# Optimization experiments

Measured on AMD Instinct MI355X. Metric: run time of the kernel, lower is better.

The kernel has to match this reference:

```python
import jax, jax.numpy as jnp
import numpy as np

DECAY = 0.97
TEMP = 0.7
EPS = 1e-6
NORM_EPS = 1e-12  # torch F.normalize default eps


def _l2norm(x, axis=-1):
    n = jnp.linalg.norm(x, axis=axis, keepdims=True)
    return x / jnp.maximum(n, NORM_EPS)


def setup_inputs() -> dict:
    key = jax.random.key(0)
    k1, k2, k3 = jax.random.split(key, 3)
    pair_embed = jax.random.normal(k1, (8, 2048, 1024), dtype=jnp.float32)
    patterns = _l2norm(jax.random.normal(k2, (4096, 1024), dtype=jnp.float32))
    usage = jax.random.uniform(k3, (4096,), dtype=jnp.float32)
    return {"pair_embed": pair_embed, "patterns": patterns, "usage": usage}


def reference(pair_embed, patterns, usage):
    G, D = patterns.shape
    flat = pair_embed.reshape(-1, D)                      # [N, D]
    queries = _l2norm(flat)
    pat_n = _l2norm(patterns)
    logits = queries @ pat_n.T                             # [N, G]
    homeostasis = jnp.log(jnp.clip(usage, EPS))
    weights = jax.nn.softmax((logits - homeostasis[None, :]) / TEMP, axis=-1)

    # Hebbian EMA update (mirrors update(); no_grad in original)
    flat_assign = weights                                  # [N, G]
    weights_sum = flat_assign.sum(axis=0)                  # [G]
    valid = weights_sum > 0
    usage_new = usage * DECAY
    usage_new = jnp.where(valid, usage_new + (1.0 - DECAY) * weights_sum, usage_new)
    updates = flat_assign.T @ flat                         # [G, D]
    updates = updates / (weights_sum[:, None] + EPS)
    blended = _l2norm(patterns * DECAY + (1.0 - DECAY) * updates)
    patterns_new = jnp.where(valid[:, None], blended, patterns)

    out_weights = weights.reshape(*pair_embed.shape[:-1], G)
    return out_weights, patterns_new, usage_new
```

## Files before the change

kernel.cpp:

```cpp
#include <hip/hip_runtime.h>
#include <stdint.h>
#include <math.h>


#define DECAY 0.97f
#define OMD 0.03f
#define INV_TEMP (1.0f / 0.7f)
#define EPS 1e-6f
#define NORM_EPS 1e-12f

constexpr int NROWS = 16384;
constexpr int DK = 1024;
constexpr int GP = 4096;

typedef unsigned short u16;
typedef __bf16 bf16x8 __attribute__((ext_vector_type(8)));
typedef float f32x4 __attribute__((ext_vector_type(4)));

__device__ inline u16 f2bf(float x) {
    union { float f; uint32_t u; } c; c.f = x;
    uint32_t r = c.u + 0x7fffu + ((c.u >> 16) & 1u);
    return (u16)(r >> 16);
}

__device__ inline void gl_lds16(const u16* g, u16* l) {
    __builtin_amdgcn_global_load_lds(
        (const __attribute__((address_space(1))) void*)g,
        (__attribute__((address_space(3))) void*)l, 16, 0, 0);
}

__global__ __launch_bounds__(256) void norm_rows_kernel(
        const float* __restrict__ in, u16* __restrict__ outn) {
    __shared__ float sred[4];
    const int row = blockIdx.x;
    const int t = threadIdx.x;
    const float4 v = ((const float4*)(in + (size_t)row * DK))[t];
    float ss = v.x * v.x + v.y * v.y + v.z * v.z + v.w * v.w;
#pragma unroll
    for (int o = 32; o > 0; o >>= 1) ss += __shfl_xor(ss, o);
    if ((t & 63) == 0) sred[t >> 6] = ss;
    __syncthreads();
    const float tot = sred[0] + sred[1] + sred[2] + sred[3];
    const float rs = 1.0f / fmaxf(sqrtf(tot), NORM_EPS);
    ushort4 o4;
    o4.x = f2bf(v.x * rs); o4.y = f2bf(v.y * rs);
    o4.z = f2bf(v.z * rs); o4.w = f2bf(v.w * rs);
    ((ushort4*)(outn + (size_t)row * DK))[t] = o4;
}

__global__ __launch_bounds__(256) void prep_scalars_kernel(
        const float* __restrict__ usage, float* __restrict__ hscaled,
        float* __restrict__ wsum, float* __restrict__ rowsum) {
    const int i = blockIdx.x * 256 + threadIdx.x;
    if (i < GP) {
        hscaled[i] = logf(fmaxf(usage[i], EPS)) * INV_TEMP;
        wsum[i] = 0.0f;
    }
    rowsum[i] = 0.0f;
}

__global__ __launch_bounds__(256) void rowinv_kernel(float* __restrict__ rowsum) {
    const int i = blockIdx.x * 256 + threadIdx.x;
    rowsum[i] = 1.0f / rowsum[i];
}

__global__ __launch_bounds__(256) void zero_kernel(float4* __restrict__ p) {
    p[(size_t)blockIdx.x * 256 + threadIdx.x] = (float4){0.f, 0.f, 0.f, 0.f};
}

__global__ __launch_bounds__(256) void transpose_f32_bf16_kernel(
        const float* __restrict__ in, u16* __restrict__ out, int R, int C) {
    __shared__ float tile[64][260];
    const int r0 = blockIdx.x * 64;
    const int c0 = blockIdx.y * 256;
    const int t = threadIdx.x;
    const int fr = t & 63;
    const int rr = t >> 6;
#pragma unroll
    for (int j = 0; j < 16; ++j) {
        const int r = rr + 4 * j;
        const float4 v = *(const float4*)(in + (size_t)(r0 + r) * C + c0 + fr * 4);
        *(float4*)&tile[r][fr * 4] = v;
    }
    __syncthreads();
    __align__(16) u16 tmp[64];
#pragma unroll
    for (int r = 0; r < 64; ++r) tmp[r] = f2bf(tile[r][t]);
    u16* op = out + (size_t)(c0 + t) * R + r0;
#pragma unroll
    for (int i = 0; i < 8; ++i) ((uint4*)op)[i] = ((const uint4*)tmp)[i];
}

__global__ __launch_bounds__(256) void scale_transpose_kernel(
        float* __restrict__ W, const float* __restrict__ invs,
        u16* __restrict__ wT, float* __restrict__ wsum) {
    __shared__ float tile[64][260];
    __shared__ float sinv[64];
    const int r0 = blockIdx.x * 64;
    const int c0 = blockIdx.y * 256;
    const int t = threadIdx.x;
    if (t < 64) sinv[t] = invs[r0 + t];
    __syncthreads();
    const int fr = t & 63;
    const int rr = t >> 6;
#pragma unroll
    for (int j = 0; j < 16; ++j) {
        const int r = rr + 4 * j;
        float4 v = *(const float4*)(W + (size_t)(r0 + r) * GP + c0 + fr * 4);
        const float s = sinv[r];
        v.x *= s; v.y *= s; v.z *= s; v.w *= s;
        *(float4*)(W + (size_t)(r0 + r) * GP + c0 + fr * 4) = v;
        *(float4*)&tile[r][fr * 4] = v;
    }
    __syncthreads();
    __align__(16) u16 tmp[64];
    float csum = 0.f;
#pragma unroll
    for (int r = 0; r < 64; ++r) {
        const float x = tile[r][t];
        csum += x;
        tmp[r] = f2bf(x);
    }
    u16* op = wT + (size_t)(c0 + t) * NROWS + r0;
#pragma unroll
    for (int i = 0; i < 8; ++i) ((uint4*)op)[i] = ((const uint4*)tmp)[i];
    atomicAdd(&wsum[c0 + t], csum);
}

template <int KSTEPS, int KLD>
__device__ inline void gemm_bt_256x256(const u16* __restrict__ A,
                                       const u16* __restrict__ B,
                                       int m0, int n0, int k0,
                                       u16* sm, f32x4 acc[8][4]) {
    constexpr int SLOT = 32768;
    constexpr int BOFF = 16384;
    const int t = threadIdx.x;
    const int lane = t & 63;
    const int wave = t >> 6;
    const int wm = (wave >> 2) * 128;
    const int wn = (wave & 3) * 64;
    const int fr = lane & 15;
    const int q8 = lane >> 4;

    const int srow = 32 * wave + (lane >> 3);
    const int soct = (lane & 7) ^ (srow & 7);
    const size_t a_base = (size_t)(m0 + srow) * KLD + k0 + soct * 8;
    const size_t b_base = (size_t)(n0 + srow) * KLD + k0 + soct * 8;

    auto STAGE = [&](int slot, int kt) {
        u16* sa = sm + slot * SLOT;
        u16* sb = sa + BOFF;
#pragma unroll
        for (int i = 0; i < 4; ++i) {
            gl_lds16(A + a_base + (size_t)(8 * i) * KLD + kt,
                     sa + (32 * wave + 8 * i) * 64);
            gl_lds16(B + b_base + (size_t)(8 * i) * KLD + kt,
                     sb + (32 * wave + 8 * i) * 64);
        }
    };

    STAGE(0, 0);
    asm volatile("s_waitcnt vmcnt(0)" ::: "memory");
    __builtin_amdgcn_sched_barrier(0);
    __builtin_amdgcn_s_barrier();
    __builtin_amdgcn_sched_barrier(0);

    int slot = 0;
#pragma unroll 1
    for (int kt = 0; kt < KSTEPS; kt += 64) {
        if (kt + 64 < KSTEPS) STAGE(slot ^ 1, kt + 64);
        const u16* sa = sm + slot * SLOT;
        const u16* sb = sa + BOFF;
#pragma unroll
        for (int ks8 = 0; ks8 < 8; ks8 += 4) {
            bf16x8 af[8], bfr[4];
#pragma unroll
            for (int f = 0; f < 8; ++f) {
                const int ra = wm + f * 16 + fr;
                af[f]  = *(const bf16x8*)(sa + ra * 64 + (((ks8 + q8) ^ (ra & 7)) * 8));
            }
#pragma unroll
            for (int f = 0; f < 4; ++f) {
                const int rb = wn + f * 16 + fr;
                bfr[f] = *(const bf16x8*)(sb + rb * 64 + (((ks8 + q8) ^ (rb & 7)) * 8));
            }
            __builtin_amdgcn_s_setprio(1);
#pragma unroll
            for (int fm = 0; fm < 8; ++fm)
#pragma unroll
                for (int fn = 0; fn < 4; ++fn)
                    acc[fm][fn] = __builtin_amdgcn_mfma_f32_16x16x32_bf16(
                        af[fm], bfr[fn], acc[fm][fn], 0, 0, 0);
            __builtin_amdgcn_s_setprio(0);
        }
        if (kt + 64 < KSTEPS) {
            asm volatile("s_waitcnt vmcnt(0)" ::: "memory");
            __builtin_amdgcn_sched_barrier(0);
            __builtin_amdgcn_s_barrier();
            __builtin_amdgcn_sched_barrier(0);
        }
        slot ^= 1;
    }
}

__global__ __launch_bounds__(512, 2) void gemm1_kernel(
        const u16* __restrict__ Q, const u16* __restrict__ P,
        const float* __restrict__ hs, float* __restrict__ Wout,
        float* __restrict__ rowsum) {
    __shared__ u16 sm[2 * 32768];
    const int bid = blockIdx.x;
    const int m0 = (bid >> 4) * 256;
    const int n0 = (bid & 15) * 256;
    f32x4 acc[8][4];
#pragma unroll
    for (int a = 0; a < 8; ++a)
#pragma unroll
        for (int b = 0; b < 4; ++b) acc[a][b] = (f32x4){0.f, 0.f, 0.f, 0.f};
    gemm_bt_256x256<DK, DK>(Q, P, m0, n0, 0, sm, acc);

    const int lane = threadIdx.x & 63;
    const int wave = threadIdx.x >> 6;
    const int wm = (wave >> 2) * 128, wn = (wave & 3) * 64;
    const int cq = lane & 15, rq = (lane >> 4) * 4;
    float hval[4];
#pragma unroll
    for (int fn = 0; fn < 4; ++fn) hval[fn] = hs[n0 + wn + fn * 16 + cq];
#pragma unroll
    for (int fm = 0; fm < 8; ++fm) {
        const int mb = m0 + wm + fm * 16 + rq;
#pragma unroll
        for (int r = 0; r < 4; ++r) {
            float rs = 0.f;
#pragma unroll
            for (int fn = 0; fn < 4; ++fn) {
                const int g = n0 + wn + fn * 16 + cq;
                const float e = __expf(acc[fm][fn][r] * INV_TEMP - hval[fn]);
                Wout[(size_t)(mb + r) * GP + g] = e;
                rs += e;
            }
#pragma unroll
            for (int o = 1; o < 16; o <<= 1) rs += __shfl_xor(rs, o);
            if (cq == 0) atomicAdd(&rowsum[mb + r], rs);
        }
    }
}

__global__ __launch_bounds__(512, 2) void gemm2_kernel(
        const u16* __restrict__ WT, const u16* __restrict__ FT,
        float* __restrict__ Upart) {
    __shared__ u16 sm[2 * 32768];
    const int bid = blockIdx.x;
    const int k0 = (bid & 3) * 4096;
    const int n0 = ((bid >> 2) & 3) * 256;
    const int m0 = (bid >> 4) * 256;
    f32x4 acc[8][4];
#pragma unroll
    for (int a = 0; a < 8; ++a)
#pragma unroll
        for (int b = 0; b < 4; ++b) acc[a][b] = (f32x4){0.f, 0.f, 0.f, 0.f};
    gemm_bt_256x256<4096, NROWS>(WT, FT, m0, n0, k0, sm, acc);

    const int lane = threadIdx.x & 63;
    const int wave = threadIdx.x >> 6;
    const int wm = (wave >> 2) * 128, wn = (wave & 3) * 64;
    const int cq = lane & 15, rq = (lane >> 4) * 4;
#pragma unroll
    for (int fn = 0; fn < 4; ++fn) {
        const int d = n0 + wn + fn * 16 + cq;
#pragma unroll
        for (int fm = 0; fm < 8; ++fm) {
            const int gb = m0 + wm + fm * 16 + rq;
#pragma unroll
            for (int r = 0; r < 4; ++r)
                atomicAdd(&Upart[(size_t)(gb + r) * DK + d], acc[fm][fn][r]);
        }
    }
}

__global__ __launch_bounds__(256) void usage_kernel(
        const float* __restrict__ usage, const float* __restrict__ wsum,
        float* __restrict__ Uout, float* __restrict__ invw) {
    const int g = blockIdx.x * 256 + threadIdx.x;
    if (g < GP) {
        const float s = wsum[g];
        Uout[g] = usage[g] * DECAY + (s > 0.f ? OMD * s : 0.f);
        invw[g] = 1.0f / (s + EPS);
    }
}

__global__ __launch_bounds__(256) void finalize_patterns_kernel(
        const float* __restrict__ patterns, const float* __restrict__ wsum,
        const float* __restrict__ invw, const float* __restrict__ Upart,
        float* __restrict__ Pout) {
    __shared__ float sred[4];
    const int g = blockIdx.x;
    const int t = threadIdx.x;
    const float iw = invw[g] * OMD;
    const float4 u4 = ((const float4*)(Upart + (size_t)g * DK))[t];
    const float4 p4 = ((const float4*)(patterns + (size_t)g * DK))[t];
    float4 b;
    b.x = DECAY * p4.x + iw * u4.x;
    b.y = DECAY * p4.y + iw * u4.y;
    b.z = DECAY * p4.z + iw * u4.z;
    b.w = DECAY * p4.w + iw * u4.w;
    float ss = b.x * b.x + b.y * b.y + b.z * b.z + b.w * b.w;
#pragma unroll
    for (int o = 32; o > 0; o >>= 1) ss += __shfl_xor(ss, o);
    if ((t & 63) == 0) sred[t >> 6] = ss;
    __syncthreads();
    const float tot = sred[0] + sred[1] + sred[2] + sred[3];
    const float rs = 1.0f / fmaxf(sqrtf(tot), NORM_EPS);
    float4 o4;
    if (wsum[g] > 0.f) {
        o4.x = b.x * rs; o4.y = b.y * rs; o4.z = b.z * rs; o4.w = b.w * rs;
    } else {
        o4 = p4;
    }
    ((float4*)(Pout + (size_t)g * DK))[t] = o4;
}

extern "C" void kernel_launch(void* const* d_in, const int* in_sizes, int n_in,
                              void* d_out, int out_size, void* d_ws, size_t ws_size,
                              hipStream_t stream) {
    const float* pair_embed = (const float*)d_in[0];
    const float* patterns   = (const float*)d_in[1];
    const float* usage      = (const float*)d_in[2];

    float* out_w = (float*)d_out;
    float* out_p = out_w + (size_t)NROWS * GP;
    float* out_u = out_p + (size_t)GP * DK;

    char* ws = (char*)d_ws;
    u16* q_bf   = (u16*)(ws);
    float* Upart = (float*)(ws);
    u16* pat_bf = (u16*)(ws + 33554432);
    u16* fT     = (u16*)(ws + 41943040);
    u16* wT     = (u16*)(ws + 75497472);
    float* hs   = (float*)(ws + 209715200);
    float* wsum = (float*)(ws + 209715200 + 16384);
    float* invw = (float*)(ws + 209715200 + 32768);
    float* rsum = (float*)(ws + 209715200 + 49152);

    prep_scalars_kernel<<<64, 256, 0, stream>>>(usage, hs, wsum, rsum);
    norm_rows_kernel<<<NROWS, 256, 0, stream>>>(pair_embed, q_bf);
    norm_rows_kernel<<<GP, 256, 0, stream>>>(patterns, pat_bf);
    {
        dim3 g(NROWS / 64, DK / 256);
        transpose_f32_bf16_kernel<<<g, 256, 0, stream>>>(pair_embed, fT, NROWS, DK);
    }
    gemm1_kernel<<<(NROWS / 256) * (GP / 256), 512, 0, stream>>>(q_bf, pat_bf, hs, out_w, rsum);
    rowinv_kernel<<<64, 256, 0, stream>>>(rsum);
    {
        dim3 g(NROWS / 64, GP / 256);
        scale_transpose_kernel<<<g, 256, 0, stream>>>(out_w, rsum, wT, wsum);
    }
    usage_kernel<<<16, 256, 0, stream>>>(usage, wsum, out_u, invw);
    zero_kernel<<<(GP * DK / 4) / 256, 256, 0, stream>>>((float4*)Upart);
    gemm2_kernel<<<4 * (GP / 256) * (DK / 256), 512, 0, stream>>>(wT, fT, Upart);
    finalize_patterns_kernel<<<GP, 256, 0, stream>>>(patterns, wsum, invw, Upart, out_p);
}
```

Measured before the change: 826.6 us.

## Split GEMM main loop into four barrier-synced LDS-load/MFMA phases

Restructures the 256x256 bf16 GEMM inner loop into four phases. Each phase loads half the A fragments (and B when needed) from LDS, synchronizes the workgroup with a barrier plus lgkmcnt wait, then issues 16 MFMAs. This halves the live A-fragment registers and aims to interleave waves' LDS reads and MFMA work, in the style of ping-pong scheduling with two blocks per CU. It adds several extra workgroup barriers per k-step, which could stall waves if the phases don't line up well.

```diff
diff --git a/kernel.cpp b/kernel.cpp
--- a/kernel.cpp
+++ b/kernel.cpp
@@ -159,6 +159,35 @@
         }
     };
 
+#define LDA4(ks8, mh) do {                                                     \
+    _Pragma("unroll")                                                          \
+    for (int f = 0; f < 4; ++f) {                                              \
+        const int ra = wm + ((mh) * 4 + f) * 16 + fr;                          \
+        af[f] = *(const bf16x8*)(sa + ra * 64 + ((((ks8) + q8) ^ (ra & 7)) * 8)); \
+    } } while (0)
+
+#define LDB4(ks8) do {                                                         \
+    _Pragma("unroll")                                                          \
+    for (int f = 0; f < 4; ++f) {                                              \
+        const int rb = wn + f * 16 + fr;                                       \
+        bfr[f] = *(const bf16x8*)(sb + rb * 64 + ((((ks8) + q8) ^ (rb & 7)) * 8)); \
+    } } while (0)
+
+#define MFMA16(mh) do {                                                        \
+    __builtin_amdgcn_s_setprio(1);                                             \
+    _Pragma("unroll")                                                          \
+    for (int f = 0; f < 4; ++f)                                                \
+        _Pragma("unroll")                                                      \
+        for (int fn = 0; fn < 4; ++fn)                                         \
+            acc[(mh) * 4 + f][fn] = __builtin_amdgcn_mfma_f32_16x16x32_bf16(   \
+                af[f], bfr[fn], acc[(mh) * 4 + f][fn], 0, 0, 0);               \
+    __builtin_amdgcn_s_setprio(0); } while (0)
+
+#define PHASE_SYNC() do {                                                      \
+    __builtin_amdgcn_s_barrier();                                              \
+    asm volatile("s_waitcnt lgkmcnt(0)" ::: "memory");                         \
+    __builtin_amdgcn_sched_barrier(0); } while (0)
+
     STAGE(0, 0);
     asm volatile("s_waitcnt vmcnt(0)" ::: "memory");
     __builtin_amdgcn_sched_barrier(0);
@@ -168,39 +197,41 @@
     int slot = 0;
 #pragma unroll 1
     for (int kt = 0; kt < KSTEPS; kt += 64) {
-        if (kt + 64 < KSTEPS) STAGE(slot ^ 1, kt + 64);
         const u16* sa = sm + slot * SLOT;
         const u16* sb = sa + BOFF;
-#pragma unroll
-        for (int ks8 = 0; ks8 < 8; ks8 += 4) {
-            bf16x8 af[8], bfr[4];
-#pragma unroll
-            for (int f = 0; f < 8; ++f) {
-                const int ra = wm + f * 16 + fr;
-                af[f]  = *(const bf16x8*)(sa + ra * 64 + (((ks8 + q8) ^ (ra & 7)) * 8));
-            }
-#pragma unroll
-            for (int f = 0; f < 4; ++f) {
-                const int rb = wn + f * 16 + fr;
-                bfr[f] = *(const bf16x8*)(sb + rb * 64 + (((ks8 + q8) ^ (rb & 7)) * 8));
-            }
-            __builtin_amdgcn_s_setprio(1);
-#pragma unroll
-            for (int fm = 0; fm < 8; ++fm)
-#pragma unroll
-                for (int fn = 0; fn < 4; ++fn)
-                    acc[fm][fn] = __builtin_amdgcn_mfma_f32_16x16x32_bf16(
-                        af[fm], bfr[fn], acc[fm][fn], 0, 0, 0);
-            __builtin_amdgcn_s_setprio(0);
-        }
-        if (kt + 64 < KSTEPS) {
-            asm volatile("s_waitcnt vmcnt(0)" ::: "memory");
-            __builtin_amdgcn_sched_barrier(0);
-            __builtin_amdgcn_s_barrier();
-            __builtin_amdgcn_sched_barrier(0);
-        }
+        const bool next = (kt + 64 < KSTEPS);
+        bf16x8 af[4], bfr[4];
+
+        if (next) STAGE(slot ^ 1, kt + 64);
+        LDA4(0, 0); LDB4(0);
+        PHASE_SYNC();
+        MFMA16(0);
+        __builtin_amdgcn_s_barrier();
+
+        LDA4(0, 1);
+        PHASE_SYNC();
+        MFMA16(1);
+        __builtin_amdgcn_s_barrier();
+
+        LDA4(4, 0); LDB4(4);
+        PHASE_SYNC();
+        MFMA16(0);
+        __builtin_amdgcn_s_barrier();
+
+        LDA4(4, 1);
+        PHASE_SYNC();
+        MFMA16(1);
+        if (next) asm volatile("s_waitcnt vmcnt(0)" ::: "memory");
+        __builtin_amdgcn_sched_barrier(0);
+        __builtin_amdgcn_s_barrier();
+        __builtin_amdgcn_sched_barrier(0);
+
         slot ^= 1;
     }
+#undef LDA4
+#undef LDB4
+#undef MFMA16
+#undef PHASE_SYNC
 }
 
 __global__ __launch_bounds__(512, 2) void gemm1_kernel(
```

Result: slower. 845.6 us (+2.3%).

## Restructure GEMM mainloop into 4-slot 32-wide K pipeline with 3-deep prefetch

Applied to the files above, without the earlier changes.

The shared 256x256 GEMM mainloop changes from a two-slot double buffer with 64-wide K tiles to a four-slot ring of 32-wide K tiles, with three stages in flight. It waits with partial vmcnt counts so only the oldest stage must land before each barrier. The LDS swizzle and staging addressing are rewritten for 32-element rows. The aim is to hide global-to-LDS latency better and drop the full vmcnt(0) drain each iteration, at the cost of twice as many barriers per K and more complex waitcnt bookkeeping.

```diff
diff --git a/kernel.cpp b/kernel.cpp
--- a/kernel.cpp
+++ b/kernel.cpp
@@ -132,8 +132,9 @@
                                        const u16* __restrict__ B,
                                        int m0, int n0, int k0,
                                        u16* sm, f32x4 acc[8][4]) {
-    constexpr int SLOT = 32768;
-    constexpr int BOFF = 16384;
+    constexpr int HSLOT = 16384;
+    constexpr int BOFF  = 8192;
+    constexpr int NH    = KSTEPS / 32;
     const int t = threadIdx.x;
     const int lane = t & 63;
     const int wave = t >> 6;
@@ -142,72 +143,74 @@
     const int fr = lane & 15;
     const int q8 = lane >> 4;
 
-    const int srow = 32 * wave + (lane >> 3);
-    const int soct = (lane & 7) ^ (srow & 7);
+    const int srow = 32 * wave + (lane >> 2);
+    const int soct = (lane & 3) ^ ((lane >> 2) & 3);
     const size_t a_base = (size_t)(m0 + srow) * KLD + k0 + soct * 8;
     const size_t b_base = (size_t)(n0 + srow) * KLD + k0 + soct * 8;
-
-    auto STAGE = [&](int slot, int kt) {
-        u16* sa = sm + slot * SLOT;
-        u16* sb = sa + BOFF;
-#pragma unroll
-        for (int i = 0; i < 4; ++i) {
-            gl_lds16(A + a_base + (size_t)(8 * i) * KLD + kt,
-                     sa + (32 * wave + 8 * i) * 64);
-            gl_lds16(B + b_base + (size_t)(8 * i) * KLD + kt,
-                     sb + (32 * wave + 8 * i) * 64);
-        }
+    u16* const sA0 = sm + (32 * wave) * 32;
+    u16* const sB0 = sm + BOFF + (32 * wave) * 32;
+
+    auto STAGEH = [&](int hh) {
+        const int so = (hh & 3) * HSLOT;
+        const size_t kadd = (size_t)hh * 32;
+        gl_lds16(A + a_base + kadd,            sA0 + so);
+        gl_lds16(A + a_base + kadd + 16 * KLD, sA0 + so + 512);
+        gl_lds16(B + b_base + kadd,            sB0 + so);
+        gl_lds16(B + b_base + kadd + 16 * KLD, sB0 + so + 512);
     };
 
-    STAGE(0, 0);
+    const int rdoff = fr * 32 + ((q8 ^ (fr & 3)) * 8);
+
+    auto COMPUTE = [&](int sl) {
+        const u16* sa = sm + sl * HSLOT + rdoff;
+        const u16* sb = sa + BOFF;
+        bf16x8 af[8], bfr[4];
+#pragma unroll
+        for (int f = 0; f < 8; ++f)
+            af[f] = *(const bf16x8*)(sa + (wm + f * 16) * 32);
+#pragma unroll
+        for (int f = 0; f < 4; ++f)
+            bfr[f] = *(const bf16x8*)(sb + (wn + f * 16) * 32);
+        asm volatile("s_waitcnt lgkmcnt(0)" ::: "memory");
+        __builtin_amdgcn_sched_barrier(0);
+        __builtin_amdgcn_s_setprio(1);
+#pragma unroll
+        for (int fm = 0; fm < 8; ++fm)
+#pragma unroll
+            for (int fn = 0; fn < 4; ++fn)
+                acc[fm][fn] = __builtin_amdgcn_mfma_f32_16x16x32_bf16(
+                    af[fm], bfr[fn], acc[fm][fn], 0, 0, 0);
+        __builtin_amdgcn_s_setprio(0);
+    };
+
+    STAGEH(0); STAGEH(1); STAGEH(2);
+
+#pragma unroll 1
+    for (int h = 0; h < NH - 2; ++h) {
+        asm volatile("s_waitcnt vmcnt(8)" ::: "memory");
+        __builtin_amdgcn_sched_barrier(0);
+        __builtin_amdgcn_s_barrier();
+        __builtin_amdgcn_sched_barrier(0);
+        if (h + 3 < NH) STAGEH(h + 3);
+        COMPUTE(h & 3);
+    }
+    asm volatile("s_waitcnt vmcnt(4)" ::: "memory");
+    __builtin_amdgcn_sched_barrier(0);
+    __builtin_amdgcn_s_barrier();
+    __builtin_amdgcn_sched_barrier(0);
+    COMPUTE((NH - 2) & 3);
     asm volatile("s_waitcnt vmcnt(0)" ::: "memory");
     __builtin_amdgcn_sched_barrier(0);
     __builtin_amdgcn_s_barrier();
     __builtin_amdgcn_sched_barrier(0);
-
-    int slot = 0;
-#pragma unroll 1
-    for (int kt = 0; kt < KSTEPS; kt += 64) {
-        if (kt + 64 < KSTEPS) STAGE(slot ^ 1, kt + 64);
-        const u16* sa = sm + slot * SLOT;
-        const u16* sb = sa + BOFF;
-#pragma unroll
-        for (int ks8 = 0; ks8 < 8; ks8 += 4) {
-            bf16x8 af[8], bfr[4];
-#pragma unroll
-            for (int f = 0; f < 8; ++f) {
-                const int ra = wm + f * 16 + fr;
-                af[f]  = *(const bf16x8*)(sa + ra * 64 + (((ks8 + q8) ^ (ra & 7)) * 8));
-            }
-#pragma unroll
-            for (int f = 0; f < 4; ++f) {
-                const int rb = wn + f * 16 + fr;
-                bfr[f] = *(const bf16x8*)(sb + rb * 64 + (((ks8 + q8) ^ (rb & 7)) * 8));
-            }
-            __builtin_amdgcn_s_setprio(1);
-#pragma unroll
-            for (int fm = 0; fm < 8; ++fm)
-#pragma unroll
-                for (int fn = 0; fn < 4; ++fn)
-                    acc[fm][fn] = __builtin_amdgcn_mfma_f32_16x16x32_bf16(
-                        af[fm], bfr[fn], acc[fm][fn], 0, 0, 0);
-            __builtin_amdgcn_s_setprio(0);
-        }
-        if (kt + 64 < KSTEPS) {
-            asm volatile("s_waitcnt vmcnt(0)" ::: "memory");
-            __builtin_amdgcn_sched_barrier(0);
-            __builtin_amdgcn_s_barrier();
-            __builtin_amdgcn_sched_barrier(0);
-        }
-        slot ^= 1;
-    }
+    COMPUTE((NH - 1) & 3);
 }
 
 __global__ __launch_bounds__(512, 2) void gemm1_kernel(
         const u16* __restrict__ Q, const u16* __restrict__ P,
         const float* __restrict__ hs, float* __restrict__ Wout,
         float* __restrict__ rowsum) {
-    __shared__ u16 sm[2 * 32768];
+    __shared__ u16 sm[4 * 16384];
     const int bid = blockIdx.x;
     const int m0 = (bid >> 4) * 256;
     const int n0 = (bid & 15) * 256;
@@ -248,7 +251,7 @@
 __global__ __launch_bounds__(512, 2) void gemm2_kernel(
         const u16* __restrict__ WT, const u16* __restrict__ FT,
         float* __restrict__ Upart) {
-    __shared__ u16 sm[2 * 32768];
+    __shared__ u16 sm[4 * 16384];
     const int bid = blockIdx.x;
     const int k0 = (bid & 3) * 4096;
     const int n0 = ((bid >> 2) & 3) * 256;
```

Result: slower. 850.5 us (+2.9%).
